# Performance work log

Hardware: AMD Instinct MI355X
Metric: run time of the kernel (lower is better)

## Reference

```python
import jax, jax.numpy as jnp
import numpy as np

N = 100000   # nodes
E = 1600000  # edges (avg degree 16)
F = 128      # input features
H = 64       # hidden_dim
C = 10       # num_classes
G = 128      # graphs in batch
EPS = 1e-5   # BatchNorm eps


def setup_inputs() -> dict:
    key = jax.random.key(0)
    ks = jax.random.split(key, 24)
    d = {}
    d['x'] = jax.random.normal(ks[0], (N, F), jnp.float32)
    d['edge_index'] = jax.random.randint(ks[1], (2, E), 0, N)
    d['batch'] = jnp.sort(jax.random.randint(ks[2], (N,), 0, G))
    # SAGEConv1: lin_l (aggregated, with bias) + lin_r (root, no bias)
    d['W1l'] = jax.random.normal(ks[3], (F, H), jnp.float32) * 0.05
    d['W1r'] = jax.random.normal(ks[4], (F, H), jnp.float32) * 0.05
    d['b1'] = jnp.zeros((H,), jnp.float32)
    # SAGEConv2
    d['W2l'] = jax.random.normal(ks[5], (H, H), jnp.float32) * 0.1
    d['W2r'] = jax.random.normal(ks[6], (H, H), jnp.float32) * 0.1
    d['b2'] = jnp.zeros((H,), jnp.float32)
    # BatchNorm (eval mode: running stats)
    for i, (kg, kb, km, kv) in enumerate([(7, 8, 9, 10), (11, 12, 13, 14), (15, 16, 17, 18)], 1):
        d[f'bn{i}_g'] = jax.random.uniform(ks[kg], (H,), jnp.float32, 0.5, 1.5)
        d[f'bn{i}_b'] = jax.random.normal(ks[kb], (H,), jnp.float32) * 0.1
        d[f'bn{i}_m'] = jax.random.normal(ks[km], (H,), jnp.float32) * 0.1
        d[f'bn{i}_v'] = jax.random.uniform(ks[kv], (H,), jnp.float32, 0.5, 1.5)
    # classifier head
    d['Wc1'] = jax.random.normal(ks[19], (H, H), jnp.float32) * 0.1
    d['bc1'] = jnp.zeros((H,), jnp.float32)
    d['Wc2'] = jax.random.normal(ks[20], (H, C), jnp.float32) * 0.1
    d['bc2'] = jnp.zeros((C,), jnp.float32)
    return d


def _bn(x, g, b, m, v):
    return (x - m) * jax.lax.rsqrt(v + EPS) * g + b


def _sage(x, src, dst, Wl, Wr, b):
    # mean aggregation of source-node features at destination nodes
    msum = jax.ops.segment_sum(x[src], dst, num_segments=N)          # [N, d]
    cnt = jax.ops.segment_sum(jnp.ones((E,), x.dtype), dst, num_segments=N)
    mean = msum / jnp.maximum(cnt, 1.0)[:, None]
    return mean @ Wl + b + x @ Wr


def reference(x, edge_index, batch,
              W1l, W1r, b1, W2l, W2r, b2,
              bn1_g, bn1_b, bn1_m, bn1_v,
              bn2_g, bn2_b, bn2_m, bn2_v,
              Wc1, bc1, bn3_g, bn3_b, bn3_m, bn3_v,
              Wc2, bc2):
    src, dst = edge_index[0], edge_index[1]
    h = _sage(x, src, dst, W1l, W1r, b1)
    h = jax.nn.relu(_bn(h, bn1_g, bn1_b, bn1_m, bn1_v))
    h = _sage(h, src, dst, W2l, W2r, b2)
    h = jax.nn.relu(_bn(h, bn2_g, bn2_b, bn2_m, bn2_v))
    # global mean pool over graphs
    gsum = jax.ops.segment_sum(h, batch, num_segments=G)             # [G, H]
    gcnt = jax.ops.segment_sum(jnp.ones((N,), h.dtype), batch, num_segments=G)
    g = gsum / jnp.maximum(gcnt, 1.0)[:, None]
    # classifier head (eval: dropout is identity)
    g = jax.nn.relu(_bn(g @ Wc1 + bc1, bn3_g, bn3_b, bn3_m, bn3_v))
    logits = g @ Wc2 + bc2
    return jax.nn.log_softmax(logits, axis=1)
```

## Files before the change

kernel.cpp:

```cpp
#include <hip/hip_runtime.h>
#include <hip/hip_bf16.h>
#include <math.h>

#define NN 100000
#define NE 1600000
#define FF 128
#define HH 64
#define CC 10
#define GG 128
#define BN_EPS 1e-5f

#define BNODES 64
#define NB 1563
#define PBLK 128
#define ECHUNK 12500
#define MHIST (NB * PBLK)
#define NSCAN 782
#define SCOL_CAP 2048

#define PNODES 16
#define POOL_BLOCKS 1563

typedef short v8bf __attribute__((ext_vector_type(8)));
typedef float v4f  __attribute__((ext_vector_type(4)));

__device__ inline ushort f2b(float x) {
    __hip_bfloat16 h = __float2bfloat16(x);
    return *reinterpret_cast<ushort*>(&h);
}
__device__ inline float b2f(ushort u) {
    return __uint_as_float(((unsigned)u) << 16);
}
__device__ inline float blo(unsigned u) { return __uint_as_float(u << 16); }
__device__ inline float bhi(unsigned u) { return __uint_as_float(u & 0xffff0000u); }

__device__ inline void sw_one(const float* __restrict__ W, ushort* __restrict__ o,
                              int t, int K) {
    const int lane = t & 63, nt = (t >> 6) & 3, ks = t >> 8;
    const int m = lane & 15, quad = lane >> 4;
#pragma unroll
    for (int j = 0; j < 8; ++j) {
        const int kk = ks * 32 + quad * 8 + j;
        const int cc = nt * 16 + m;
        o[t * 8 + j] = f2b(W[kk * 64 + cc]);
    }
}

__global__ __launch_bounds__(256) void prep_kernel(const float* __restrict__ W1l,
                                                   const float* __restrict__ W1r,
                                                   const float* __restrict__ W2l,
                                                   const float* __restrict__ W2r,
                                                   ushort* __restrict__ w1ls,
                                                   ushort* __restrict__ w1rs,
                                                   ushort* __restrict__ w2ls,
                                                   ushort* __restrict__ w2rs,
                                                   float* __restrict__ gz) {
    const int t = blockIdx.x * 256 + threadIdx.x;
    if (t < 1024) {
        sw_one(W1l, w1ls, t, FF);
        sw_one(W1r, w1rs, t, FF);
    } else if (t < 1536) {
        sw_one(W2l, w2ls, t - 1024, HH);
        sw_one(W2r, w2rs, t - 1024, HH);
    } else {
        for (int i = t - 1536; i < GG * 64 + GG; i += 512) gz[i] = 0.f;
    }
}

template<int K, int TPB, bool AF32>
__global__ __launch_bounds__(256) void gemm_mfma(const void* __restrict__ Xv,
                                                 const ushort* __restrict__ Bl,
                                                 const ushort* __restrict__ Br,
                                                 ushort* __restrict__ Yl,
                                                 ushort* __restrict__ Yr) {
    constexpr int KS = K / 32;
    const int lane  = threadIdx.x & 63;
    const int wave  = threadIdx.x >> 6;
    const int nhalf = wave & 1;
    const int rsub  = wave >> 1;
    const int m = lane & 15, quad = lane >> 4;

    v8bf bl[KS][2], br[KS][2];
#pragma unroll
    for (int ks = 0; ks < KS; ++ks)
#pragma unroll
        for (int nt = 0; nt < 2; ++nt) {
            const int nti = nhalf * 2 + nt;
            bl[ks][nt] = *(const v8bf*)(Bl + ((size_t)(ks * 4 + nti) * 64 + lane) * 8);
            br[ks][nt] = *(const v8bf*)(Br + ((size_t)(ks * 4 + nti) * 64 + lane) * 8);
        }

    for (int it = 0; it < TPB; ++it) {
        const int bt = blockIdx.x * TPB + it;
        const int row0 = bt * 32 + rsub * 16;
        if (row0 >= NN) return;
        const v4f z = {0.f, 0.f, 0.f, 0.f};
        v4f accl[2] = {z, z}, accr[2] = {z, z};
#pragma unroll
        for (int ks = 0; ks < KS; ++ks) {
            v8bf a;
            if (AF32) {
                const float* xrow = (const float*)Xv + (size_t)(row0 + m) * K + quad * 8 + ks * 32;
                const float4 a0 = *(const float4*)(xrow);
                const float4 a1 = *(const float4*)(xrow + 4);
                a[0] = (short)f2b(a0.x); a[1] = (short)f2b(a0.y);
                a[2] = (short)f2b(a0.z); a[3] = (short)f2b(a0.w);
                a[4] = (short)f2b(a1.x); a[5] = (short)f2b(a1.y);
                a[6] = (short)f2b(a1.z); a[7] = (short)f2b(a1.w);
            } else {
                const ushort* xrow = (const ushort*)Xv + (size_t)(row0 + m) * K + quad * 8 + ks * 32;
                a = *(const v8bf*)xrow;
            }
#pragma unroll
            for (int nt = 0; nt < 2; ++nt) {
                accl[nt] = __builtin_amdgcn_mfma_f32_16x16x32_bf16(a, bl[ks][nt], accl[nt], 0, 0, 0);
                accr[nt] = __builtin_amdgcn_mfma_f32_16x16x32_bf16(a, br[ks][nt], accr[nt], 0, 0, 0);
            }
        }
#pragma unroll
        for (int nt = 0; nt < 2; ++nt) {
            const int cc = nhalf * 32 + nt * 16 + m;
#pragma unroll
            for (int r = 0; r < 4; ++r) {
                const size_t off = (size_t)(row0 + quad * 4 + r) * 64 + cc;
                Yl[off] = f2b(accl[nt][r]);
                Yr[off] = f2b(accr[nt][r]);
            }
        }
    }
}

__global__ __launch_bounds__(1024) void edge_hist(const int* __restrict__ dst,
                                                  int* __restrict__ hist) {
    __shared__ int h[NB];
    for (int i = threadIdx.x; i < NB; i += 1024) h[i] = 0;
    __syncthreads();
    const int e0 = blockIdx.x * ECHUNK;
    for (int e = e0 + threadIdx.x; e < e0 + ECHUNK; e += 1024)
        atomicAdd(&h[dst[e] >> 6], 1);
    __syncthreads();
    for (int i = threadIdx.x; i < NB; i += 1024)
        hist[i * PBLK + blockIdx.x] = h[i];
}

__global__ __launch_bounds__(256) void scan_block(const int* __restrict__ cnt,
                                                  int* __restrict__ rp,
                                                  int* __restrict__ bsum) {
    __shared__ int ws[4];
    const int tid = threadIdx.x;
    const int lane = tid & 63, wv = tid >> 6;
    const int i = blockIdx.x * 256 + tid;
    const int v = (i < MHIST) ? cnt[i] : 0;
    int inc = v;
#pragma unroll
    for (int off = 1; off < 64; off <<= 1) {
        int t = __shfl_up(inc, off, 64);
        if (lane >= off) inc += t;
    }
    if (lane == 63) ws[wv] = inc;
    __syncthreads();
    int wbase = 0;
#pragma unroll
    for (int w = 0; w < 4; ++w) wbase += (w < wv) ? ws[w] : 0;
    if (i < MHIST) rp[i] = wbase + inc - v;
    if (tid == 255) bsum[blockIdx.x] = wbase + inc;
}

__global__ __launch_bounds__(256) void scan_bsums(const int* __restrict__ bsum,
                                                  int* __restrict__ boff) {
    __shared__ int ws[4];
    const int tid = threadIdx.x;
    const int lane = tid & 63, wv = tid >> 6;
    int v[4];
    int tot = 0;
#pragma unroll
    for (int j = 0; j < 4; ++j) {
        const int idx = tid * 4 + j;
        v[j] = (idx < NSCAN) ? bsum[idx] : 0;
        tot += v[j];
    }
    int inc = tot;
#pragma unroll
    for (int off = 1; off < 64; off <<= 1) {
        int t = __shfl_up(inc, off, 64);
        if (lane >= off) inc += t;
    }
    if (lane == 63) ws[wv] = inc;
    __syncthreads();
    int wbase = 0;
#pragma unroll
    for (int w = 0; w < 4; ++w) wbase += (w < wv) ? ws[w] : 0;
    int run = wbase + inc - tot;
#pragma unroll
    for (int j = 0; j < 4; ++j) {
        const int idx = tid * 4 + j;
        if (idx < NSCAN) boff[idx] = run;
        run += v[j];
    }
}

__global__ __launch_bounds__(1024) void edge_scatter(const int* __restrict__ src,
                                                     const int* __restrict__ dst,
                                                     const int* __restrict__ hist,
                                                     const int* __restrict__ goffs,
                                                     const int* __restrict__ boff,
                                                     int* __restrict__ pairs) {
    __shared__ int sv[ECHUNK];
    __shared__ int sd[ECHUNK];
    __shared__ int sfill[NB];
    __shared__ int sdelta[NB];
    __shared__ int wsum[16];
    const int tid = threadIdx.x;
    const int lane = tid & 63, wv = tid >> 6;
    const int p = blockIdx.x;

    int c0 = 0, c1 = 0, g0 = 0, g1 = 0;
    const int i0 = 2 * tid, i1 = 2 * tid + 1;
    if (i0 < NB) {
        const int idx = i0 * PBLK + p;
        c0 = hist[idx];
        g0 = goffs[idx] + boff[idx >> 8];
    }
    if (i1 < NB) {
        const int idx = i1 * PBLK + p;
        c1 = hist[idx];
        g1 = goffs[idx] + boff[idx >> 8];
    }
    const int tv = c0 + c1;
    int inc = tv;
#pragma unroll
    for (int off = 1; off < 64; off <<= 1) {
        int t = __shfl_up(inc, off, 64);
        if (lane >= off) inc += t;
    }
    if (lane == 63) wsum[wv] = inc;
    __syncthreads();
    int wbase = 0;
#pragma unroll
    for (int w = 0; w < 16; ++w) wbase += (w < wv) ? wsum[w] : 0;
    const int excl = wbase + inc - tv;
    if (i0 < NB) { sfill[i0] = excl;      sdelta[i0] = g0 - excl; }
    if (i1 < NB) { sfill[i1] = excl + c0; sdelta[i1] = g1 - (excl + c0); }
    __syncthreads();

    const int e0 = p * ECHUNK;
    for (int e = e0 + tid; e < e0 + ECHUNK; e += 1024) {
        const int s = src[e];
        const int d = dst[e];
        const int b = d >> 6;
        const int local = atomicAdd(&sfill[b], 1);
        sv[local] = (s << 6) | (d & (BNODES - 1));
        sd[local] = local + sdelta[b];
    }
    __syncthreads();

    for (int j = tid; j < ECHUNK; j += 1024) {
        pairs[sd[j]] = sv[j];
    }
}

__global__ __launch_bounds__(256) void spmm_sorted(const int* __restrict__ goffs,
                                                   const int* __restrict__ boff,
                                                   const int* __restrict__ pairs,
                                                   const ushort* __restrict__ Yl,
                                                   const ushort* __restrict__ Yr,
                                                   const float* __restrict__ bias,
                                                   const float* __restrict__ bng,
                                                   const float* __restrict__ bnb,
                                                   const float* __restrict__ bnm,
                                                   const float* __restrict__ bnv,
                                                   ushort* __restrict__ outp) {
    __shared__ int scol[SCOL_CAP];
    __shared__ int deg[BNODES];
    __shared__ int loffs[BNODES];
    __shared__ int fill[BNODES];
    const int tid = threadIdx.x;
    const int b = blockIdx.x;

    if (tid < BNODES) { deg[tid] = 0; fill[tid] = 0; }
    __syncthreads();

    const int beg = goffs[b * PBLK] + boff[b >> 1];
    int end = (b == NB - 1) ? NE : goffs[(b + 1) * PBLK] + boff[(b + 1) >> 1];
    if (end - beg > SCOL_CAP) end = beg + SCOL_CAP;

    int pv[8];
    int npv = 0;
    for (int i = beg + tid; i < end; i += 256) {
        const int v = pairs[i];
        pv[npv++] = v;
        atomicAdd(&deg[v & (BNODES - 1)], 1);
    }
    __syncthreads();

    if (tid < BNODES) loffs[tid] = deg[tid];
    __syncthreads();
    for (int s = 1; s < BNODES; s <<= 1) {
        int v = 0;
        if (tid < BNODES && tid >= s) v = loffs[tid - s];
        __syncthreads();
        if (tid < BNODES) loffs[tid] += v;
        __syncthreads();
    }

    for (int j = 0; j < npv; ++j) {
        const int v = pv[j];
        const int dl = v & (BNODES - 1);
        const int pos = (loffs[dl] - deg[dl]) + atomicAdd(&fill[dl], 1);
        scol[pos] = v >> 6;
    }
    __syncthreads();

    const int wv = tid >> 6, lane = tid & 63;
    const int grp = lane >> 3, subl = lane & 7;

    float biasj[8], scj[8], mj[8], bbj[8];
#pragma unroll
    for (int j = 0; j < 8; ++j) {
        const int ch = subl * 8 + j;
        biasj[j] = bias[ch];
        scj[j] = bng[ch] * rsqrtf(bnv[ch] + BN_EPS);
        mj[j] = bnm[ch];
        bbj[j] = bnb[ch];
    }

    for (int i = 0; i < 2; ++i) {
        const int nl = wv * 16 + i * 8 + grp;
        const int node = b * BNODES + nl;
        if (node >= NN) continue;
        const int dg = deg[nl];
        const int nbeg = loffs[nl] - dg;
        const int nend = nbeg + dg;
        float a[8] = {0.f, 0.f, 0.f, 0.f, 0.f, 0.f, 0.f, 0.f};
        float c[8] = {0.f, 0.f, 0.f, 0.f, 0.f, 0.f, 0.f, 0.f};
        int e = nbeg;
        for (; e + 1 < nend; e += 2) {
            const int s0 = scol[e];
            const int s1 = scol[e + 1];
            const uint4 r0 = *(const uint4*)(Yl + (size_t)s0 * 64 + subl * 8);
            const uint4 r1 = *(const uint4*)(Yl + (size_t)s1 * 64 + subl * 8);
            a[0] += blo(r0.x); a[1] += bhi(r0.x); a[2] += blo(r0.y); a[3] += bhi(r0.y);
            a[4] += blo(r0.z); a[5] += bhi(r0.z); a[6] += blo(r0.w); a[7] += bhi(r0.w);
            c[0] += blo(r1.x); c[1] += bhi(r1.x); c[2] += blo(r1.y); c[3] += bhi(r1.y);
            c[4] += blo(r1.z); c[5] += bhi(r1.z); c[6] += blo(r1.w); c[7] += bhi(r1.w);
        }
        if (e < nend) {
            const int s0 = scol[e];
            const uint4 r0 = *(const uint4*)(Yl + (size_t)s0 * 64 + subl * 8);
            a[0] += blo(r0.x); a[1] += bhi(r0.x); a[2] += blo(r0.y); a[3] += bhi(r0.y);
            a[4] += blo(r0.z); a[5] += bhi(r0.z); a[6] += blo(r0.w); a[7] += bhi(r0.w);
        }
        const float inv = 1.0f / fmaxf((float)dg, 1.0f);
        const uint4 yr = *(const uint4*)(Yr + (size_t)node * 64 + subl * 8);
        float hj[8];
        hj[0] = (a[0] + c[0]) * inv + biasj[0] + blo(yr.x);
        hj[1] = (a[1] + c[1]) * inv + biasj[1] + bhi(yr.x);
        hj[2] = (a[2] + c[2]) * inv + biasj[2] + blo(yr.y);
        hj[3] = (a[3] + c[3]) * inv + biasj[3] + bhi(yr.y);
        hj[4] = (a[4] + c[4]) * inv + biasj[4] + blo(yr.z);
        hj[5] = (a[5] + c[5]) * inv + biasj[5] + bhi(yr.z);
        hj[6] = (a[6] + c[6]) * inv + biasj[6] + blo(yr.w);
        hj[7] = (a[7] + c[7]) * inv + biasj[7] + bhi(yr.w);
        unsigned ow[4];
#pragma unroll
        for (int j = 0; j < 4; ++j) {
            const float o0 = fmaxf((hj[2 * j] - mj[2 * j]) * scj[2 * j] + bbj[2 * j], 0.0f);
            const float o1 = fmaxf((hj[2 * j + 1] - mj[2 * j + 1]) * scj[2 * j + 1] + bbj[2 * j + 1], 0.0f);
            ow[j] = (unsigned)f2b(o0) | ((unsigned)f2b(o1) << 16);
        }
        uint4 o;
        o.x = ow[0]; o.y = ow[1]; o.z = ow[2]; o.w = ow[3];
        *(uint4*)(outp + (size_t)node * 64 + subl * 8) = o;
    }
}

__global__ __launch_bounds__(256) void pool_seg(const ushort* __restrict__ h,
                                                const int* __restrict__ batch,
                                                float* __restrict__ gsum,
                                                float* __restrict__ gcnt) {
    const int wave = blockIdx.x * 4 + (threadIdx.x >> 6);
    const int lane = threadIdx.x & 63;
    const int n0 = wave * PNODES;
    if (n0 >= NN) return;
    const int n1 = (n0 + PNODES < NN) ? n0 + PNODES : NN;
    int g = batch[n0];
    float acc = 0.f, c = 0.f;
#pragma unroll 4
    for (int n = n0; n < n1; ++n) {
        const int b = batch[n];
        if (b != g) {
            atomicAdd(&gsum[g * 64 + lane], acc);
            if (lane == 0) atomicAdd(&gcnt[g], c);
            acc = 0.f; c = 0.f; g = b;
        }
        acc += b2f(h[(size_t)n * 64 + lane]);
        c += 1.0f;
    }
    atomicAdd(&gsum[g * 64 + lane], acc);
    if (lane == 0) atomicAdd(&gcnt[g], c);
}

__global__ __launch_bounds__(64) void head_kernel(const float* __restrict__ gsum,
                                                  const float* __restrict__ gcnt,
                                                  const float* __restrict__ Wc1,
                                                  const float* __restrict__ bc1,
                                                  const float* __restrict__ g3,
                                                  const float* __restrict__ b3,
                                                  const float* __restrict__ m3,
                                                  const float* __restrict__ v3,
                                                  const float* __restrict__ Wc2,
                                                  const float* __restrict__ bc2,
                                                  float* __restrict__ out) {
    __shared__ float sg[64];
    __shared__ float st[64];
    __shared__ float sl[10];
    __shared__ float sls;
    const int b = blockIdx.x;
    const int c = threadIdx.x;
    sg[c] = gsum[b * 64 + c] / fmaxf(gcnt[b], 1.0f);
    __syncthreads();
    float acc = bc1[c];
#pragma unroll
    for (int k = 0; k < 64; ++k) acc += sg[k] * Wc1[k * 64 + c];
    const float sc = g3[c] * rsqrtf(v3[c] + BN_EPS);
    st[c] = fmaxf((acc - m3[c]) * sc + b3[c], 0.0f);
    __syncthreads();
    if (c < CC) {
        float lg = bc2[c];
#pragma unroll
        for (int k = 0; k < 64; ++k) lg += st[k] * Wc2[k * CC + c];
        sl[c] = lg;
    }
    __syncthreads();
    if (c == 0) {
        float mx = sl[0];
        for (int i = 1; i < CC; ++i) mx = fmaxf(mx, sl[i]);
        float s = 0.f;
        for (int i = 0; i < CC; ++i) s += expf(sl[i] - mx);
        sls = mx + logf(s);
    }
    __syncthreads();
    if (c < CC) out[b * CC + c] = sl[c] - sls;
}

extern "C" void kernel_launch(void* const* d_in, const int* in_sizes, int n_in,
                              void* d_out, int out_size, void* d_ws, size_t ws_size,
                              hipStream_t stream) {
    const float* x    = (const float*)d_in[0];
    const int*   ei   = (const int*)d_in[1];
    const int*   batch= (const int*)d_in[2];
    const float* W1l  = (const float*)d_in[3];
    const float* W1r  = (const float*)d_in[4];
    const float* b1   = (const float*)d_in[5];
    const float* W2l  = (const float*)d_in[6];
    const float* W2r  = (const float*)d_in[7];
    const float* b2   = (const float*)d_in[8];
    const float* bn1g = (const float*)d_in[9];
    const float* bn1b = (const float*)d_in[10];
    const float* bn1m = (const float*)d_in[11];
    const float* bn1v = (const float*)d_in[12];
    const float* bn2g = (const float*)d_in[13];
    const float* bn2b = (const float*)d_in[14];
    const float* bn2m = (const float*)d_in[15];
    const float* bn2v = (const float*)d_in[16];
    const float* bn3g = (const float*)d_in[17];
    const float* bn3b = (const float*)d_in[18];
    const float* bn3m = (const float*)d_in[19];
    const float* bn3v = (const float*)d_in[20];
    const float* Wc1  = (const float*)d_in[21];
    const float* bc1  = (const float*)d_in[22];
    const float* Wc2  = (const float*)d_in[23];
    const float* bc2  = (const float*)d_in[24];
    float* out = (float*)d_out;

    const int* src = ei;
    const int* dst = ei + NE;

    char* p = (char*)d_ws;
    ushort* yl   = (ushort*)p;                 p += (size_t)NN * 64 * 2;
    ushort* yr   = (ushort*)p;                 p += (size_t)NN * 64 * 2;
    ushort* hbuf = (ushort*)p;                 p += (size_t)NN * 64 * 2;
    int*    pairs= (int*)p;                    p += (size_t)NE * 4;
    int*    hist = (int*)p;                    p += (size_t)MHIST * 4;
    int*    goffs= (int*)p;                    p += (size_t)MHIST * 4;
    int*    bsum = (int*)p;                    p += 1024 * 4;
    int*    boff = (int*)p;                    p += 1024 * 4;
    ushort* w1ls = (ushort*)p;                 p += (size_t)FF * 64 * 2;
    ushort* w1rs = (ushort*)p;                 p += (size_t)FF * 64 * 2;
    ushort* w2ls = (ushort*)p;                 p += (size_t)HH * 64 * 2;
    ushort* w2rs = (ushort*)p;                 p += (size_t)HH * 64 * 2;
    float* gsum  = (float*)p;                  p += (size_t)GG * 64 * 4;
    float* gcnt  = gsum + GG * 64;             p += (size_t)GG * 4;

    edge_hist<<<PBLK, 1024, 0, stream>>>(dst, hist);
    scan_block<<<NSCAN, 256, 0, stream>>>(hist, goffs, bsum);
    scan_bsums<<<1, 256, 0, stream>>>(bsum, boff);
    edge_scatter<<<PBLK, 1024, 0, stream>>>(src, dst, hist, goffs, boff, pairs);

    prep_kernel<<<8, 256, 0, stream>>>(W1l, W1r, W2l, W2r, w1ls, w1rs, w2ls, w2rs, gsum);

    gemm_mfma<FF, 2, true><<<1563, 256, 0, stream>>>((const void*)x, w1ls, w1rs, yl, yr);
    spmm_sorted<<<NB, 256, 0, stream>>>(goffs, boff, pairs, yl, yr, b1,
                                        bn1g, bn1b, bn1m, bn1v, hbuf);

    gemm_mfma<HH, 2, false><<<1563, 256, 0, stream>>>((const void*)hbuf, w2ls, w2rs, yl, yr);
    spmm_sorted<<<NB, 256, 0, stream>>>(goffs, boff, pairs, yl, yr, b2,
                                        bn2g, bn2b, bn2m, bn2v, hbuf);

    pool_seg<<<POOL_BLOCKS, 256, 0, stream>>>(hbuf, batch, gsum, gcnt);
    head_kernel<<<GG, 64, 0, stream>>>(gsum, gcnt, Wc1, bc1,
                                       bn3g, bn3b, bn3m, bn3v, Wc2, bc2, out);
}
```

Baseline: 286.0 us.

## Fuse global mean pooling into second SpMM and weight prep into histogram

Drops the separate pool_seg kernel. The second SpMM now accumulates relu'd node features into per-block shared-memory buckets for up to four graphs and flushes them to global sums with atomics, so the hidden buffer is no longer written and re-read. Weight swizzling and zeroing of the pool accumulators move into two extra blocks of edge_hist, removing another launch. It also swaps the LDS degree scan for a wave shuffle scan and unrolls the gather loop by four. The cost is many shared-memory float atomics per node in the fused kernel, a global-atomic fallback when a block spans more than four graphs, and a float summation order that is no longer deterministic.

Result: no change. 287.3 us (+0.5%).

```diff
diff --git a/kernel.cpp b/kernel.cpp
--- a/kernel.cpp
+++ b/kernel.cpp
@@ -18,9 +18,6 @@
 #define NSCAN 782
 #define SCOL_CAP 2048
 
-#define PNODES 16
-#define POOL_BLOCKS 1563
-
 typedef short v8bf __attribute__((ext_vector_type(8)));
 typedef float v4f  __attribute__((ext_vector_type(4)));
 
@@ -33,6 +30,11 @@
 }
 __device__ inline float blo(unsigned u) { return __uint_as_float(u << 16); }
 __device__ inline float bhi(unsigned u) { return __uint_as_float(u & 0xffff0000u); }
+
+__device__ inline void acc8(float* a, const uint4 r) {
+    a[0] += blo(r.x); a[1] += bhi(r.x); a[2] += blo(r.y); a[3] += bhi(r.y);
+    a[4] += blo(r.z); a[5] += bhi(r.z); a[6] += blo(r.w); a[7] += bhi(r.w);
+}
 
 __device__ inline void sw_one(const float* __restrict__ W, ushort* __restrict__ o,
                               int t, int K) {
@@ -43,27 +45,6 @@
         const int kk = ks * 32 + quad * 8 + j;
         const int cc = nt * 16 + m;
         o[t * 8 + j] = f2b(W[kk * 64 + cc]);
-    }
-}
-
-__global__ __launch_bounds__(256) void prep_kernel(const float* __restrict__ W1l,
-                                                   const float* __restrict__ W1r,
-                                                   const float* __restrict__ W2l,
-                                                   const float* __restrict__ W2r,
-                                                   ushort* __restrict__ w1ls,
-                                                   ushort* __restrict__ w1rs,
-                                                   ushort* __restrict__ w2ls,
-                                                   ushort* __restrict__ w2rs,
-                                                   float* __restrict__ gz) {
-    const int t = blockIdx.x * 256 + threadIdx.x;
-    if (t < 1024) {
-        sw_one(W1l, w1ls, t, FF);
-        sw_one(W1r, w1rs, t, FF);
-    } else if (t < 1536) {
-        sw_one(W2l, w2ls, t - 1024, HH);
-        sw_one(W2r, w2rs, t - 1024, HH);
-    } else {
-        for (int i = t - 1536; i < GG * 64 + GG; i += 512) gz[i] = 0.f;
     }
 }
 
@@ -131,7 +112,31 @@
 }
 
 __global__ __launch_bounds__(1024) void edge_hist(const int* __restrict__ dst,
-                                                  int* __restrict__ hist) {
+                                                  int* __restrict__ hist,
+                                                  const float* __restrict__ W1l,
+                                                  const float* __restrict__ W1r,
+                                                  const float* __restrict__ W2l,
+                                                  const float* __restrict__ W2r,
+                                                  ushort* __restrict__ w1ls,
+                                                  ushort* __restrict__ w1rs,
+                                                  ushort* __restrict__ w2ls,
+                                                  ushort* __restrict__ w2rs,
+                                                  float* __restrict__ gz) {
+    if (blockIdx.x >= PBLK) {
+        const int t = threadIdx.x;
+        if (blockIdx.x == PBLK) {
+            sw_one(W1l, w1ls, t, FF);
+            sw_one(W1r, w1rs, t, FF);
+        } else {
+            if (t < 512) {
+                sw_one(W2l, w2ls, t, HH);
+                sw_one(W2r, w2rs, t, HH);
+            } else {
+                for (int i = t - 512; i < GG * 64 + GG; i += 512) gz[i] = 0.f;
+            }
+        }
+        return;
+    }
     __shared__ int h[NB];
     for (int i = threadIdx.x; i < NB; i += 1024) h[i] = 0;
     __syncthreads();
@@ -259,6 +264,7 @@
     }
 }
 
+template<bool POOL>
 __global__ __launch_bounds__(256) void spmm_sorted(const int* __restrict__ goffs,
                                                    const int* __restrict__ boff,
                                                    const int* __restrict__ pairs,
@@ -269,15 +275,26 @@
                                                    const float* __restrict__ bnb,
                                                    const float* __restrict__ bnm,
                                                    const float* __restrict__ bnv,
-                                                   ushort* __restrict__ outp) {
+                                                   ushort* __restrict__ outp,
+                                                   const int* __restrict__ batch,
+                                                   float* __restrict__ gsum,
+                                                   float* __restrict__ gcnt) {
     __shared__ int scol[SCOL_CAP];
     __shared__ int deg[BNODES];
     __shared__ int loffs[BNODES];
     __shared__ int fill[BNODES];
+    __shared__ float pbuf[4][64];
+    __shared__ float pcnt[4];
+    __shared__ int g0s;
     const int tid = threadIdx.x;
     const int b = blockIdx.x;
 
     if (tid < BNODES) { deg[tid] = 0; fill[tid] = 0; }
+    if (POOL) {
+        pbuf[tid >> 6][tid & 63] = 0.f;
+        if (tid < 4) pcnt[tid] = 0.f;
+        if (tid == 0) g0s = batch[b * BNODES];
+    }
     __syncthreads();
 
     const int beg = goffs[b * PBLK] + boff[b >> 1];
@@ -293,15 +310,17 @@
     }
     __syncthreads();
 
-    if (tid < BNODES) loffs[tid] = deg[tid];
-    __syncthreads();
-    for (int s = 1; s < BNODES; s <<= 1) {
-        int v = 0;
-        if (tid < BNODES && tid >= s) v = loffs[tid - s];
-        __syncthreads();
-        if (tid < BNODES) loffs[tid] += v;
-        __syncthreads();
-    }
+    if (tid < BNODES) {
+        const int v = deg[tid];
+        int inc = v;
+#pragma unroll
+        for (int s = 1; s < 64; s <<= 1) {
+            int t = __shfl_up(inc, s, 64);
+            if (tid >= s) inc += t;
+        }
+        loffs[tid] = inc;
+    }
+    __syncthreads();
 
     for (int j = 0; j < npv; ++j) {
         const int v = pv[j];
@@ -334,21 +353,25 @@
         float a[8] = {0.f, 0.f, 0.f, 0.f, 0.f, 0.f, 0.f, 0.f};
         float c[8] = {0.f, 0.f, 0.f, 0.f, 0.f, 0.f, 0.f, 0.f};
         int e = nbeg;
-        for (; e + 1 < nend; e += 2) {
-            const int s0 = scol[e];
-            const int s1 = scol[e + 1];
+        for (; e + 3 < nend; e += 4) {
+            const int s0 = scol[e], s1 = scol[e + 1], s2 = scol[e + 2], s3 = scol[e + 3];
             const uint4 r0 = *(const uint4*)(Yl + (size_t)s0 * 64 + subl * 8);
             const uint4 r1 = *(const uint4*)(Yl + (size_t)s1 * 64 + subl * 8);
-            a[0] += blo(r0.x); a[1] += bhi(r0.x); a[2] += blo(r0.y); a[3] += bhi(r0.y);
-            a[4] += blo(r0.z); a[5] += bhi(r0.z); a[6] += blo(r0.w); a[7] += bhi(r0.w);
-            c[0] += blo(r1.x); c[1] += bhi(r1.x); c[2] += blo(r1.y); c[3] += bhi(r1.y);
-            c[4] += blo(r1.z); c[5] += bhi(r1.z); c[6] += blo(r1.w); c[7] += bhi(r1.w);
+            const uint4 r2 = *(const uint4*)(Yl + (size_t)s2 * 64 + subl * 8);
+            const uint4 r3 = *(const uint4*)(Yl + (size_t)s3 * 64 + subl * 8);
+            acc8(a, r0); acc8(c, r1); acc8(a, r2); acc8(c, r3);
+        }
+        if (e + 1 < nend) {
+            const int s0 = scol[e], s1 = scol[e + 1];
+            const uint4 r0 = *(const uint4*)(Yl + (size_t)s0 * 64 + subl * 8);
+            const uint4 r1 = *(const uint4*)(Yl + (size_t)s1 * 64 + subl * 8);
+            acc8(a, r0); acc8(c, r1);
+            e += 2;
         }
         if (e < nend) {
             const int s0 = scol[e];
             const uint4 r0 = *(const uint4*)(Yl + (size_t)s0 * 64 + subl * 8);
-            a[0] += blo(r0.x); a[1] += bhi(r0.x); a[2] += blo(r0.y); a[3] += bhi(r0.y);
-            a[4] += blo(r0.z); a[5] += bhi(r0.z); a[6] += blo(r0.w); a[7] += bhi(r0.w);
+            acc8(a, r0);
         }
         const float inv = 1.0f / fmaxf((float)dg, 1.0f);
         const uint4 yr = *(const uint4*)(Yr + (size_t)node * 64 + subl * 8);
@@ -361,43 +384,45 @@
         hj[5] = (a[5] + c[5]) * inv + biasj[5] + bhi(yr.z);
         hj[6] = (a[6] + c[6]) * inv + biasj[6] + blo(yr.w);
         hj[7] = (a[7] + c[7]) * inv + biasj[7] + bhi(yr.w);
-        unsigned ow[4];
-#pragma unroll
-        for (int j = 0; j < 4; ++j) {
-            const float o0 = fmaxf((hj[2 * j] - mj[2 * j]) * scj[2 * j] + bbj[2 * j], 0.0f);
-            const float o1 = fmaxf((hj[2 * j + 1] - mj[2 * j + 1]) * scj[2 * j + 1] + bbj[2 * j + 1], 0.0f);
-            ow[j] = (unsigned)f2b(o0) | ((unsigned)f2b(o1) << 16);
-        }
-        uint4 o;
-        o.x = ow[0]; o.y = ow[1]; o.z = ow[2]; o.w = ow[3];
-        *(uint4*)(outp + (size_t)node * 64 + subl * 8) = o;
-    }
-}
-
-__global__ __launch_bounds__(256) void pool_seg(const ushort* __restrict__ h,
-                                                const int* __restrict__ batch,
-                                                float* __restrict__ gsum,
-                                                float* __restrict__ gcnt) {
-    const int wave = blockIdx.x * 4 + (threadIdx.x >> 6);
-    const int lane = threadIdx.x & 63;
-    const int n0 = wave * PNODES;
-    if (n0 >= NN) return;
-    const int n1 = (n0 + PNODES < NN) ? n0 + PNODES : NN;
-    int g = batch[n0];
-    float acc = 0.f, c = 0.f;
-#pragma unroll 4
-    for (int n = n0; n < n1; ++n) {
-        const int b = batch[n];
-        if (b != g) {
-            atomicAdd(&gsum[g * 64 + lane], acc);
-            if (lane == 0) atomicAdd(&gcnt[g], c);
-            acc = 0.f; c = 0.f; g = b;
-        }
-        acc += b2f(h[(size_t)n * 64 + lane]);
-        c += 1.0f;
-    }
-    atomicAdd(&gsum[g * 64 + lane], acc);
-    if (lane == 0) atomicAdd(&gcnt[g], c);
+        float o[8];
+#pragma unroll
+        for (int j = 0; j < 8; ++j)
+            o[j] = fmaxf((hj[j] - mj[j]) * scj[j] + bbj[j], 0.0f);
+        if (!POOL) {
+            unsigned ow[4];
+#pragma unroll
+            for (int j = 0; j < 4; ++j)
+                ow[j] = (unsigned)f2b(o[2 * j]) | ((unsigned)f2b(o[2 * j + 1]) << 16);
+            uint4 ov;
+            ov.x = ow[0]; ov.y = ow[1]; ov.z = ow[2]; ov.w = ow[3];
+            *(uint4*)(outp + (size_t)node * 64 + subl * 8) = ov;
+        } else {
+            const int g = batch[node];
+            const int gi = g - g0s;
+            if (gi < 4) {
+#pragma unroll
+                for (int j = 0; j < 8; ++j) atomicAdd(&pbuf[gi][subl * 8 + j], o[j]);
+                if (subl == 0) atomicAdd(&pcnt[gi], 1.0f);
+            } else {
+#pragma unroll
+                for (int j = 0; j < 8; ++j) atomicAdd(&gsum[g * 64 + subl * 8 + j], o[j]);
+                if (subl == 0) atomicAdd(&gcnt[g], 1.0f);
+            }
+        }
+    }
+    if (POOL) {
+        __syncthreads();
+        const int q = tid >> 6, ch = tid & 63;
+        const int g = g0s + q;
+        if (g < GG) {
+            const float v = pbuf[q][ch];
+            if (v != 0.f) atomicAdd(&gsum[g * 64 + ch], v);
+        }
+        if (tid < 4) {
+            const int gq = g0s + tid;
+            if (gq < GG && pcnt[tid] > 0.f) atomicAdd(&gcnt[gq], pcnt[tid]);
+        }
+    }
 }
 
 __global__ __launch_bounds__(64) void head_kernel(const float* __restrict__ gsum,
@@ -492,22 +517,22 @@
     float* gsum  = (float*)p;                  p += (size_t)GG * 64 * 4;
     float* gcnt  = gsum + GG * 64;             p += (size_t)GG * 4;
 
-    edge_hist<<<PBLK, 1024, 0, stream>>>(dst, hist);
+    edge_hist<<<PBLK + 2, 1024, 0, stream>>>(dst, hist, W1l, W1r, W2l, W2r,
+                                             w1ls, w1rs, w2ls, w2rs, gsum);
     scan_block<<<NSCAN, 256, 0, stream>>>(hist, goffs, bsum);
     scan_bsums<<<1, 256, 0, stream>>>(bsum, boff);
     edge_scatter<<<PBLK, 1024, 0, stream>>>(src, dst, hist, goffs, boff, pairs);
 
-    prep_kernel<<<8, 256, 0, stream>>>(W1l, W1r, W2l, W2r, w1ls, w1rs, w2ls, w2rs, gsum);
-
     gemm_mfma<FF, 2, true><<<1563, 256, 0, stream>>>((const void*)x, w1ls, w1rs, yl, yr);
-    spmm_sorted<<<NB, 256, 0, stream>>>(goffs, boff, pairs, yl, yr, b1,
-                                        bn1g, bn1b, bn1m, bn1v, hbuf);
+    spmm_sorted<false><<<NB, 256, 0, stream>>>(goffs, boff, pairs, yl, yr, b1,
+                                               bn1g, bn1b, bn1m, bn1v, hbuf,
+                                               batch, gsum, gcnt);
 
     gemm_mfma<HH, 2, false><<<1563, 256, 0, stream>>>((const void*)hbuf, w2ls, w2rs, yl, yr);
-    spmm_sorted<<<NB, 256, 0, stream>>>(goffs, boff, pairs, yl, yr, b2,
-                                        bn2g, bn2b, bn2m, bn2v, hbuf);
-
-    pool_seg<<<POOL_BLOCKS, 256, 0, stream>>>(hbuf, batch, gsum, gcnt);
+    spmm_sorted<true><<<NB, 256, 0, stream>>>(goffs, boff, pairs, yl, yr, b2,
+                                              bn2g, bn2b, bn2m, bn2v, hbuf,
+                                              batch, gsum, gcnt);
+
     head_kernel<<<GG, 64, 0, stream>>>(gsum, gcnt, Wc1, bc1,
                                        bn3g, bn3b, bn3m, bn3v, Wc2, bc2, out);
 }
```
